# Optimization experiments

Measured on AMD Instinct MI355X. Metric: run time of the kernel, lower is better.

## Reference

```python
import jax, jax.numpy as jnp
import numpy as np

T, D, H = 32768, 64, 128  # timesteps, input_size, hidden_size

def setup_inputs() -> dict:
    key = jax.random.key(0)
    ks = jax.random.split(key, 13)
    s_ih = 1.0 / np.sqrt(H)
    def u(k, shape):
        return jax.random.uniform(k, shape, jnp.float32, -s_ih, s_ih)
    return {
        "X": jax.random.normal(ks[0], (T, 1, D), jnp.float32),
        "W_ih": u(ks[1], (4 * H, D)),
        "W_hh": u(ks[2], (4 * H, H)),
        "b_ih": u(ks[3], (4 * H,)),
        "b_hh": u(ks[4], (4 * H,)),
        "W1": u(ks[5], (11, H)), "b1": u(ks[6], (11,)),
        "W2": u(ks[7], (2, H)),  "b2": u(ks[8], (2,)),
        "W3": u(ks[9], (1, H)),  "b3": u(ks[10], (1,)),
        "W4": u(ks[11], (1, H)), "b4": u(ks[12], (1,)),
    }

def reference(X, W_ih, W_hh, b_ih, b_hh, W1, b1, W2, b2, W3, b3, W4, b4):
    # LSTMCell recurrence over T steps, batch=1 (masks are identity: Dropout(p=0) on ones)
    def cell(carry, x):
        h, c = carry  # [1,H]
        gates = x @ W_ih.T + b_ih + h @ W_hh.T + b_hh  # [1,4H]
        i, f, g, o = jnp.split(gates, 4, axis=-1)
        c2 = jax.nn.sigmoid(f) * c + jax.nn.sigmoid(i) * jnp.tanh(g)
        h2 = jax.nn.sigmoid(o) * jnp.tanh(c2)
        return (h2, c2), h2

    h0 = jnp.zeros((1, H), X.dtype)
    c0 = jnp.zeros((1, H), X.dtype)
    _, hs = jax.lax.scan(cell, (h0, c0), X)  # hs: [T,1,H]
    out = hs[:, 0, :]  # squeeze -> [T,H]

    # MtFc head: 4 small linears on the same features
    step = out @ W1.T + b1        # [T,11]
    experience = out @ W2.T + b2  # [T,2]
    rsd = out @ W3.T + b3         # [T,1]
    s = out @ W4.T + b4           # [T,1]
    return (step, experience, rsd, s)
```

## Files before the change

kernel.cpp:

```cpp
#include <hip/hip_runtime.h>
#include <hip/hip_bf16.h>
#include <cstdint>
#include <cstddef>

#define T_STEPS 32768
#define DD 64
#define HH 128
#define GG 512

#define OFF_EXP 360448
#define OFF_RSD 425984
#define OFF_S   458752

typedef __attribute__((ext_vector_type(2))) _Float16 half2v;

__device__ __forceinline__ int   f2i(float x) { union { float f; int i; } u; u.f = x; return u.i; }
__device__ __forceinline__ float i2f(int x)   { union { int i; float f; } u; u.i = x; return u.f; }

template<int CTRL>
__device__ __forceinline__ float qdpp(float v) {
    return i2f(__builtin_amdgcn_mov_dpp(f2i(v), CTRL, 0xf, 0xf, true));
}
#define QP_XOR1 0xB1
#define QP_XOR2 0x4E
#define QP_BC0  0x00
#define QP_BC1  0x55
#define QP_BC2  0xAA
#define QP_BC3  0xFF

__device__ __forceinline__ float dot2(unsigned w, unsigned h, float acc) {
    union { unsigned u; half2v h; } a, b;
    a.u = w; b.u = h;
    return __builtin_amdgcn_fdot2(a.h, b.h, acc, false);
}
__device__ __forceinline__ unsigned packh2(float x, float y) {
    union { half2v h; unsigned u; } c;
    c.h[0] = (_Float16)x; c.h[1] = (_Float16)y;
    return c.u;
}
__device__ __forceinline__ float exp2_f(float x) {
    float r; asm("v_exp_f32 %0, %1" : "=v"(r) : "v"(x)); return r;
}

__global__ __launch_bounds__(512, 2) void pregate_kernel(
    const float* __restrict__ X, const float* __restrict__ W_ih,
    const float* __restrict__ b_ih, const float* __restrict__ b_hh,
    float* __restrict__ P, int t0, int nrows)
{
    __shared__ __align__(16) float xs[DD];
    const int j = threadIdx.x;
    const int grow = (j & 3) * HH + (j >> 2);

    float w[DD];
    const float4* wv = reinterpret_cast<const float4*>(W_ih + (size_t)grow * DD);
#pragma unroll
    for (int k = 0; k < DD / 4; ++k) {
        float4 v = wv[k];
        w[4*k+0] = v.x; w[4*k+1] = v.y; w[4*k+2] = v.z; w[4*k+3] = v.w;
    }
    const float bias = b_ih[grow] + b_hh[grow];

    const int rpb = (nrows + gridDim.x - 1) / gridDim.x;
    const int r0  = blockIdx.x * rpb;
    const int r1  = (r0 + rpb < nrows) ? (r0 + rpb) : nrows;

    for (int r = r0; r < r1; ++r) {
        const int t = t0 + r;
        if (j < DD) xs[j] = X[(size_t)t * DD + j];
        __syncthreads();
        float acc = bias;
        const float4* xv = reinterpret_cast<const float4*>(xs);
#pragma unroll
        for (int k = 0; k < DD / 4; ++k) {
            float4 v = xv[k];
            acc += v.x*w[4*k+0] + v.y*w[4*k+1] + v.z*w[4*k+2] + v.w*w[4*k+3];
        }
        P[(size_t)r * GG + j] = acc;
        __syncthreads();
    }
}

__global__ __launch_bounds__(512, 2) void lstm_seq_kernel(
    const float* __restrict__ P, const float* __restrict__ W_hh,
    float* __restrict__ hist, float* __restrict__ state,
    int t0, int C)
{
    __shared__ __align__(16) _Float16 hh2[2][HH];

    const int j    = threadIdx.x;
    const int cell = j >> 2;
    const int q    = j & 3;

    unsigned w2[64];
#pragma unroll
    for (int g = 0; g < 4; ++g) {
        const float* wr = W_hh + (size_t)(g * HH + cell) * HH + 32 * q;
#pragma unroll
        for (int k = 0; k < 16; ++k)
            w2[g * 16 + k] = packh2(wr[2*k], wr[2*k+1]);
    }
#pragma unroll
    for (int i = 0; i < 64; ++i) asm volatile("" : "+v"(w2[i]));

    const bool  isg = (q == 2);
    const float sA  = isg ?  2.885390082f : -1.442695041f;
    const float sB  = isg ? -2.0f : 1.0f;
    const float sC  = isg ?  1.0f : 0.0f;

    float c = 0.0f;
    if (t0 != 0) c = state[HH + cell];
    if (j < HH) hh2[0][j] = (_Float16)((t0 != 0) ? state[j] : 0.0f);
    __syncthreads();

    const _Float16* hb0 = &hh2[0][32 * q];
    const _Float16* hb1 = &hh2[1][32 * q];

    float pcq = P[j];
    float pn1 = (C > 1) ? P[GG + j] : 0.0f;
    float hn  = 0.0f;

#pragma unroll 1
    for (int r = 0; r < C; ++r) {
        const uint4* hp = reinterpret_cast<const uint4*>((r & 1) ? hb1 : hb0);
        const uint4 h0 = hp[0], h1 = hp[1], h2 = hp[2], h3 = hp[3];

        float pn2 = 0.0f;
        if (r + 2 < C) pn2 = P[(size_t)(r + 2) * GG + j];

        float p0 = 0.f, p1 = 0.f, p2 = 0.f, p3 = 0.f;
#define DOTK(hx, k) \
        p0 = dot2(w2[k],      hx, p0); p1 = dot2(w2[16 + k], hx, p1); \
        p2 = dot2(w2[32 + k], hx, p2); p3 = dot2(w2[48 + k], hx, p3);
        DOTK(h0.x, 0)  DOTK(h0.y, 1)  DOTK(h0.z, 2)  DOTK(h0.w, 3)
        DOTK(h1.x, 4)  DOTK(h1.y, 5)  DOTK(h1.z, 6)  DOTK(h1.w, 7)
        DOTK(h2.x, 8)  DOTK(h2.y, 9)  DOTK(h2.z, 10) DOTK(h2.w, 11)
        DOTK(h3.x, 12) DOTK(h3.y, 13) DOTK(h3.z, 14) DOTK(h3.w, 15)
#undef DOTK

        float ka = (q & 2) ? p2 : p0;
        float kb = (q & 2) ? p3 : p1;
        float sa = (q & 2) ? p0 : p2;
        float sb = (q & 2) ? p1 : p3;
        ka += qdpp<QP_XOR2>(sa);
        kb += qdpp<QP_XOR2>(sb);
        float own = (q & 1) ? kb : ka;
        float snd = (q & 1) ? ka : kb;
        own += qdpp<QP_XOR1>(snd);

        const float pre = own + pcq;
        const float t   = __builtin_amdgcn_rcpf(1.0f + exp2_f(pre * sA));
        const float a   = __builtin_fmaf(t, sB, sC);

        const float ai = qdpp<QP_BC0>(a);
        const float af = qdpp<QP_BC1>(a);
        const float ag = qdpp<QP_BC2>(a);
        const float ao = qdpp<QP_BC3>(a);

        c = __builtin_fmaf(af, c, ai * ag);
        const float tc = __builtin_amdgcn_rcpf(1.0f + exp2_f(c * 2.885390082f));
        hn = ao * __builtin_fmaf(tc, -2.0f, 1.0f);

        if (q == 0) {
            hh2[(r & 1) ^ 1][cell] = (_Float16)hn;
            hist[(size_t)r * HH + cell] = hn;
        }

        pcq = pn1; pn1 = pn2;

        asm volatile("s_waitcnt lgkmcnt(0)" ::: "memory");
        __builtin_amdgcn_s_barrier();
        __builtin_amdgcn_sched_barrier(0);
    }

    if (q == 0) {
        state[cell]      = hn;
        state[HH + cell] = c;
    }
}

__global__ __launch_bounds__(256, 4) void heads_kernel(
    const float* __restrict__ hist,
    const float* __restrict__ W1, const float* __restrict__ b1,
    const float* __restrict__ W2, const float* __restrict__ b2,
    const float* __restrict__ W3, const float* __restrict__ b3,
    const float* __restrict__ W4, const float* __restrict__ b4,
    float* __restrict__ out, int t0, int C)
{
    const int idx = blockIdx.x * 256 + threadIdx.x;
    const int tr  = idx >> 4;
    const int oi  = idx & 15;
    if (tr >= C || oi >= 15) return;

    const float* wrow;
    float bias;
    if (oi < 11)       { wrow = W1 + oi * HH;        bias = b1[oi]; }
    else if (oi < 13)  { wrow = W2 + (oi - 11) * HH; bias = b2[oi - 11]; }
    else if (oi == 13) { wrow = W3;                  bias = b3[0]; }
    else               { wrow = W4;                  bias = b4[0]; }

    const float4* h4 = reinterpret_cast<const float4*>(hist + (size_t)tr * HH);
    const float4* w4 = reinterpret_cast<const float4*>(wrow);
    float s = bias;
#pragma unroll
    for (int k = 0; k < HH / 4; ++k) {
        float4 hv = h4[k];
        float4 wv = w4[k];
        s += hv.x*wv.x + hv.y*wv.y + hv.z*wv.z + hv.w*wv.w;
    }
    const int t = t0 + tr;
    if (oi < 11)       out[(size_t)t * 11 + oi] = s;
    else if (oi < 13)  out[OFF_EXP + (size_t)t * 2 + (oi - 11)] = s;
    else if (oi == 13) out[OFF_RSD + t] = s;
    else               out[OFF_S + t] = s;
}

extern "C" void kernel_launch(void* const* d_in, const int* in_sizes, int n_in,
                              void* d_out, int out_size, void* d_ws, size_t ws_size,
                              hipStream_t stream)
{
    const float* X    = (const float*)d_in[0];
    const float* W_ih = (const float*)d_in[1];
    const float* W_hh = (const float*)d_in[2];
    const float* b_ih = (const float*)d_in[3];
    const float* b_hh = (const float*)d_in[4];
    const float* W1   = (const float*)d_in[5];
    const float* b1   = (const float*)d_in[6];
    const float* W2   = (const float*)d_in[7];
    const float* b2   = (const float*)d_in[8];
    const float* W3   = (const float*)d_in[9];
    const float* b3   = (const float*)d_in[10];
    const float* W4   = (const float*)d_in[11];
    const float* b4   = (const float*)d_in[12];

    float* out   = (float*)d_out;
    float* state = (float*)d_ws;

    size_t avail = (ws_size > 1024) ? (ws_size - 1024) / 2560 : 0;
    int C = (avail >= (size_t)T_STEPS) ? T_STEPS : (int)avail;
    if (C < 1) C = 1;
    float* hist = state + 256;
    float* P    = hist + (size_t)C * HH;

    for (int t0 = 0; t0 < T_STEPS; t0 += C) {
        const int Cc = (C < T_STEPS - t0) ? C : (T_STEPS - t0);
        const int nb = (Cc < 512) ? Cc : 512;
        pregate_kernel<<<nb, 512, 0, stream>>>(X, W_ih, b_ih, b_hh, P, t0, Cc);
        lstm_seq_kernel<<<1, 512, 0, stream>>>(P, W_hh, hist, state, t0, Cc);
        heads_kernel<<<(Cc * 16 + 255) / 256, 256, 0, stream>>>(
            hist, W1, b1, W2, b2, W3, b3, W4, b4, out, t0, Cc);
    }
}
```

Measured before the change: 17.14 ms.

## Compute LSTM recurrent matvec with MFMA 16x16x32 f16 instead of fdot2

Replaces the per-thread fdot2 recurrent matvec and DPP cross-lane reductions with MFMA 16x16x32 f16 instructions, using the broadcast h vector as the A operand and register-resident W_hh fragments as B. Gate rows are reordered in both the pregate kernel and the recurrent kernel to match the MFMA output layout. Gate activations go through LDS so 16 lanes per wave can finish the cell update. This aims to cut the serial per-step latency of the matvec. The cost is a wasted 16-row MFMA on a single vector, plus an extra LDS round trip and a waitcnt each step.

```diff
diff --git a/kernel.cpp b/kernel.cpp
--- a/kernel.cpp
+++ b/kernel.cpp
@@ -12,34 +12,15 @@
 #define OFF_RSD 425984
 #define OFF_S   458752
 
-typedef __attribute__((ext_vector_type(2))) _Float16 half2v;
-
-__device__ __forceinline__ int   f2i(float x) { union { float f; int i; } u; u.f = x; return u.i; }
-__device__ __forceinline__ float i2f(int x)   { union { int i; float f; } u; u.i = x; return u.f; }
-
-template<int CTRL>
-__device__ __forceinline__ float qdpp(float v) {
-    return i2f(__builtin_amdgcn_mov_dpp(f2i(v), CTRL, 0xf, 0xf, true));
-}
-#define QP_XOR1 0xB1
-#define QP_XOR2 0x4E
-#define QP_BC0  0x00
-#define QP_BC1  0x55
-#define QP_BC2  0xAA
-#define QP_BC3  0xFF
-
-__device__ __forceinline__ float dot2(unsigned w, unsigned h, float acc) {
-    union { unsigned u; half2v h; } a, b;
-    a.u = w; b.u = h;
-    return __builtin_amdgcn_fdot2(a.h, b.h, acc, false);
-}
-__device__ __forceinline__ unsigned packh2(float x, float y) {
-    union { half2v h; unsigned u; } c;
-    c.h[0] = (_Float16)x; c.h[1] = (_Float16)y;
-    return c.u;
-}
+typedef __attribute__((ext_vector_type(8))) _Float16 half8;
+typedef __attribute__((ext_vector_type(4))) float f32x4;
+
 __device__ __forceinline__ float exp2_f(float x) {
     float r; asm("v_exp_f32 %0, %1" : "=v"(r) : "v"(x)); return r;
+}
+
+__device__ __forceinline__ int grow_of(int j) {
+    return (j & 3) * HH + (j >> 6) * 16 + ((j >> 4) & 3) * 4 + ((j & 15) >> 2);
 }
 
 __global__ __launch_bounds__(512, 2) void pregate_kernel(
@@ -49,7 +30,7 @@
 {
     __shared__ __align__(16) float xs[DD];
     const int j = threadIdx.x;
-    const int grow = (j & 3) * HH + (j >> 2);
+    const int grow = grow_of(j);
 
     float w[DD];
     const float4* wv = reinterpret_cast<const float4*>(W_ih + (size_t)grow * DD);
@@ -86,85 +67,103 @@
     int t0, int C)
 {
     __shared__ __align__(16) _Float16 hh2[2][HH];
+    __shared__ __align__(16) float gate_lds[GG];
 
     const int j    = threadIdx.x;
-    const int cell = j >> 2;
-    const int q    = j & 3;
-
-    unsigned w2[64];
-#pragma unroll
-    for (int g = 0; g < 4; ++g) {
-        const float* wr = W_hh + (size_t)(g * HH + cell) * HH + 32 * q;
-#pragma unroll
-        for (int k = 0; k < 16; ++k)
-            w2[g * 16 + k] = packh2(wr[2*k], wr[2*k+1]);
-    }
-#pragma unroll
-    for (int i = 0; i < 64; ++i) asm volatile("" : "+v"(w2[i]));
-
-    const bool  isg = (q == 2);
+    const int w    = j >> 6;
+    const int l    = j & 63;
+    const int col  = l & 15;
+    const int kgrp = l >> 4;
+    const int gt   = l & 3;
+
+    half8 wf[4][4];
+#pragma unroll
+    for (int mt = 0; mt < 4; ++mt) {
+        const int growB = gt * HH + 16 * w + 4 * mt + (col >> 2);
+        const float* wr = W_hh + (size_t)growB * HH + 8 * kgrp;
+#pragma unroll
+        for (int kt = 0; kt < 4; ++kt) {
+            const float* wp = wr + 32 * kt;
+            float4 w0 = *reinterpret_cast<const float4*>(wp);
+            float4 w1 = *reinterpret_cast<const float4*>(wp + 4);
+            half8 hf;
+            hf[0] = (_Float16)w0.x; hf[1] = (_Float16)w0.y;
+            hf[2] = (_Float16)w0.z; hf[3] = (_Float16)w0.w;
+            hf[4] = (_Float16)w1.x; hf[5] = (_Float16)w1.y;
+            hf[6] = (_Float16)w1.z; hf[7] = (_Float16)w1.w;
+            wf[mt][kt] = hf;
+        }
+    }
+
+    const bool  isg = (gt == 2);
     const float sA  = isg ?  2.885390082f : -1.442695041f;
     const float sB  = isg ? -2.0f : 1.0f;
     const float sC  = isg ?  1.0f : 0.0f;
-
+    const bool  b0  = (kgrp & 1) != 0;
+    const bool  b1  = (kgrp & 2) != 0;
+
+    const int mycell = 16 * w + l;
     float c = 0.0f;
-    if (t0 != 0) c = state[HH + cell];
+    if (t0 != 0 && l < 16) c = state[HH + mycell];
     if (j < HH) hh2[0][j] = (_Float16)((t0 != 0) ? state[j] : 0.0f);
     __syncthreads();
 
-    const _Float16* hb0 = &hh2[0][32 * q];
-    const _Float16* hb1 = &hh2[1][32 * q];
-
     float pcq = P[j];
     float pn1 = (C > 1) ? P[GG + j] : 0.0f;
-    float hn  = 0.0f;
+    const float* pp = P + 2 * (size_t)GG + j;
+    float* hw = hist + mycell;
+    float hn = 0.0f;
+    const f32x4 Z = {0.0f, 0.0f, 0.0f, 0.0f};
 
 #pragma unroll 1
     for (int r = 0; r < C; ++r) {
-        const uint4* hp = reinterpret_cast<const uint4*>((r & 1) ? hb1 : hb0);
-        const uint4 h0 = hp[0], h1 = hp[1], h2 = hp[2], h3 = hp[3];
+        const _Float16* hb = &hh2[r & 1][8 * kgrp];
+        const half8 a0 = *reinterpret_cast<const half8*>(hb);
+        const half8 a1 = *reinterpret_cast<const half8*>(hb + 32);
+        const half8 a2 = *reinterpret_cast<const half8*>(hb + 64);
+        const half8 a3 = *reinterpret_cast<const half8*>(hb + 96);
 
         float pn2 = 0.0f;
-        if (r + 2 < C) pn2 = P[(size_t)(r + 2) * GG + j];
-
-        float p0 = 0.f, p1 = 0.f, p2 = 0.f, p3 = 0.f;
-#define DOTK(hx, k) \
-        p0 = dot2(w2[k],      hx, p0); p1 = dot2(w2[16 + k], hx, p1); \
-        p2 = dot2(w2[32 + k], hx, p2); p3 = dot2(w2[48 + k], hx, p3);
-        DOTK(h0.x, 0)  DOTK(h0.y, 1)  DOTK(h0.z, 2)  DOTK(h0.w, 3)
-        DOTK(h1.x, 4)  DOTK(h1.y, 5)  DOTK(h1.z, 6)  DOTK(h1.w, 7)
-        DOTK(h2.x, 8)  DOTK(h2.y, 9)  DOTK(h2.z, 10) DOTK(h2.w, 11)
-        DOTK(h3.x, 12) DOTK(h3.y, 13) DOTK(h3.z, 14) DOTK(h3.w, 15)
-#undef DOTK
-
-        float ka = (q & 2) ? p2 : p0;
-        float kb = (q & 2) ? p3 : p1;
-        float sa = (q & 2) ? p0 : p2;
-        float sb = (q & 2) ? p1 : p3;
-        ka += qdpp<QP_XOR2>(sa);
-        kb += qdpp<QP_XOR2>(sb);
-        float own = (q & 1) ? kb : ka;
-        float snd = (q & 1) ? ka : kb;
-        own += qdpp<QP_XOR1>(snd);
-
-        const float pre = own + pcq;
+        if (r + 2 < C) pn2 = *pp;
+        pp += GG;
+
+        f32x4 q0 = __builtin_amdgcn_mfma_f32_16x16x32_f16(a0, wf[0][0], Z, 0, 0, 0);
+        f32x4 q1 = __builtin_amdgcn_mfma_f32_16x16x32_f16(a0, wf[1][0], Z, 0, 0, 0);
+        f32x4 q2 = __builtin_amdgcn_mfma_f32_16x16x32_f16(a0, wf[2][0], Z, 0, 0, 0);
+        f32x4 q3 = __builtin_amdgcn_mfma_f32_16x16x32_f16(a0, wf[3][0], Z, 0, 0, 0);
+        q0 = __builtin_amdgcn_mfma_f32_16x16x32_f16(a1, wf[0][1], q0, 0, 0, 0);
+        q1 = __builtin_amdgcn_mfma_f32_16x16x32_f16(a1, wf[1][1], q1, 0, 0, 0);
+        q2 = __builtin_amdgcn_mfma_f32_16x16x32_f16(a1, wf[2][1], q2, 0, 0, 0);
+        q3 = __builtin_amdgcn_mfma_f32_16x16x32_f16(a1, wf[3][1], q3, 0, 0, 0);
+        q0 = __builtin_amdgcn_mfma_f32_16x16x32_f16(a2, wf[0][2], q0, 0, 0, 0);
+        q1 = __builtin_amdgcn_mfma_f32_16x16x32_f16(a2, wf[1][2], q1, 0, 0, 0);
+        q2 = __builtin_amdgcn_mfma_f32_16x16x32_f16(a2, wf[2][2], q2, 0, 0, 0);
+        q3 = __builtin_amdgcn_mfma_f32_16x16x32_f16(a2, wf[3][2], q3, 0, 0, 0);
+        q0 = __builtin_amdgcn_mfma_f32_16x16x32_f16(a3, wf[0][3], q0, 0, 0, 0);
+        q1 = __builtin_amdgcn_mfma_f32_16x16x32_f16(a3, wf[1][3], q1, 0, 0, 0);
+        q2 = __builtin_amdgcn_mfma_f32_16x16x32_f16(a3, wf[2][3], q2, 0, 0, 0);
+        q3 = __builtin_amdgcn_mfma_f32_16x16x32_f16(a3, wf[3][3], q3, 0, 0, 0);
+
+        const float s01  = b0 ? q1[0] : q0[0];
+        const float s23  = b0 ? q3[0] : q2[0];
+        const float ssum = b1 ? s23 : s01;
+
+        const float pre = ssum + pcq;
         const float t   = __builtin_amdgcn_rcpf(1.0f + exp2_f(pre * sA));
         const float a   = __builtin_fmaf(t, sB, sC);
 
-        const float ai = qdpp<QP_BC0>(a);
-        const float af = qdpp<QP_BC1>(a);
-        const float ag = qdpp<QP_BC2>(a);
-        const float ao = qdpp<QP_BC3>(a);
-
-        c = __builtin_fmaf(af, c, ai * ag);
-        const float tc = __builtin_amdgcn_rcpf(1.0f + exp2_f(c * 2.885390082f));
-        hn = ao * __builtin_fmaf(tc, -2.0f, 1.0f);
-
-        if (q == 0) {
-            hh2[(r & 1) ^ 1][cell] = (_Float16)hn;
-            hist[(size_t)r * HH + cell] = hn;
+        gate_lds[64 * w + 16 * kgrp + col] = a;
+        asm volatile("s_waitcnt lgkmcnt(0)" ::: "memory");
+
+        if (l < 16) {
+            const f32x4 g4 = *reinterpret_cast<const f32x4*>(&gate_lds[64 * w + 4 * l]);
+            c = __builtin_fmaf(g4[1], c, g4[0] * g4[2]);
+            const float tc = __builtin_amdgcn_rcpf(1.0f + exp2_f(c * 2.885390082f));
+            hn = g4[3] * __builtin_fmaf(tc, -2.0f, 1.0f);
+            hh2[(r & 1) ^ 1][mycell] = (_Float16)hn;
+            *hw = hn;
         }
-
+        hw += HH;
         pcq = pn1; pn1 = pn2;
 
         asm volatile("s_waitcnt lgkmcnt(0)" ::: "memory");
@@ -172,9 +171,9 @@
         __builtin_amdgcn_sched_barrier(0);
     }
 
-    if (q == 0) {
-        state[cell]      = hn;
-        state[HH + cell] = c;
+    if (l < 16) {
+        state[mycell]      = hn;
+        state[HH + mycell] = c;
     }
 }
 
```

Result: faster. 16.58 ms, median of 2 (-3.3%).
